# Optimization experiments

Hardware: AMD Instinct MI355X
Metric: run time of the kernel (lower is better)

Reference implementation:

```python
import jax, jax.numpy as jnp
import numpy as np


def setup_inputs() -> dict:
    key = jax.random.key(0)
    k1, k2, k3, k4 = jax.random.split(key, 4)
    b, c, h, w = 4, 256, 64, 64
    Fq_l = jax.random.normal(k1, (b, c, h, w), dtype=jnp.float32)
    Fp_l = jax.random.normal(k2, (b, c, h, w), dtype=jnp.float32)
    # 1x1 conv: weight [out=c//2, in=c], bias [c//2]
    W = jax.random.normal(k3, (c // 2, c), dtype=jnp.float32) * (1.0 / np.sqrt(c))
    bias = jax.random.normal(k4, (c // 2,), dtype=jnp.float32) * 0.01
    return {"Fq_l": Fq_l, "Fp_l": Fp_l, "W": W, "bias": bias}


def reference(Fq_l, Fp_l, W, bias):
    b, c, h, w = Fq_l.shape
    hw = h * w
    # 1x1 conv == per-pixel linear projection
    q = jnp.einsum('oc,bchw->bohw', W, Fq_l) + bias[None, :, None, None]
    p = jnp.einsum('oc,bchw->bohw', W, Fp_l) + bias[None, :, None, None]
    qf = q.reshape(b, -1, hw)  # [b, c/2, hw]
    pf = p.reshape(b, -1, hw)
    qf = qf / jnp.linalg.norm(qf, axis=1, keepdims=True)
    pf = pf / jnp.linalg.norm(pf, axis=1, keepdims=True)
    # cosine similarity, [b, hw, hw]
    sim = jnp.einsum('bcn,bcm->bnm', qf, pf)
    idx = jnp.argmax(sim, axis=-1)  # [b, hw]
    Fp_flat = Fp_l.reshape(b, c, hw)
    aligned = jnp.take_along_axis(Fp_flat, idx[:, None, :], axis=2)  # [b, c, hw]
    return aligned.reshape(b, c, h, w)
```

## Files before the change

kernel.cpp:

```cpp
#include <hip/hip_runtime.h>

#define HW 4096
#define LCAP 1536

typedef short bf16x8 __attribute__((ext_vector_type(8)));
typedef float f32x16 __attribute__((ext_vector_type(16)));

__device__ __forceinline__ ushort f2bf_rne(float f) {
    unsigned u = __float_as_uint(f);
    return (ushort)((u + 0x7FFFu + ((u >> 16) & 1u)) >> 16);
}

__global__ __launch_bounds__(256) void transpose_w_kernel(
    const float* __restrict__ Wm, float* __restrict__ Wt)
{
    const int o = blockIdx.x;
    const int c = threadIdx.x;
    Wt[c * 128 + o] = Wm[o * 256 + c];
}

__global__ __launch_bounds__(256) void proj_kernel(
    const float* __restrict__ Fq, const float* __restrict__ Fp,
    const float* __restrict__ Wt, const float* __restrict__ bias,
    float* __restrict__ Qt, float* __restrict__ Pt,
    ushort* __restrict__ Qpk, ushort* __restrict__ Ppk,
    float* __restrict__ qnorm)
{
    __shared__ float Ws[64][128];
    __shared__ float Xs[64][128];
    __shared__ float psum[16][137];

    const int tid = threadIdx.x;
    const int z  = blockIdx.z;
    const float* __restrict__ X = z ? Fp : Fq;
    const int b  = blockIdx.y;
    const int n0 = blockIdx.x * 128;
    const int og = tid >> 4;
    const int ng = tid & 15;

    float acc[8][8];
    #pragma unroll
    for (int i = 0; i < 8; ++i)
        #pragma unroll
        for (int j = 0; j < 8; ++j) acc[i][j] = 0.f;

    for (int cc = 0; cc < 4; ++cc) {
        __syncthreads();
        {
            const float4* src = (const float4*)(Wt + (size_t)cc * 64 * 128);
            float4* dst = (float4*)Ws;
            #pragma unroll
            for (int it = 0; it < 8; ++it) dst[it * 256 + tid] = src[it * 256 + tid];
        }
        #pragma unroll
        for (int it = 0; it < 8; ++it) {
            int f = it * 256 + tid;
            int r = f >> 5, n4 = f & 31;
            *(float4*)&Xs[r][n4 * 4] =
                *(const float4*)&X[(size_t)(b * 256 + cc * 64 + r) * HW + n0 + n4 * 4];
        }
        __syncthreads();

        for (int r = 0; r < 64; ++r) {
            float4 w0 = *(const float4*)&Ws[r][og * 8];
            float4 w1 = *(const float4*)&Ws[r][og * 8 + 4];
            float4 x0 = *(const float4*)&Xs[r][ng * 8];
            float4 x1 = *(const float4*)&Xs[r][ng * 8 + 4];
            float wa[8] = {w0.x, w0.y, w0.z, w0.w, w1.x, w1.y, w1.z, w1.w};
            float xa[8] = {x0.x, x0.y, x0.z, x0.w, x1.x, x1.y, x1.z, x1.w};
            #pragma unroll
            for (int i = 0; i < 8; ++i)
                #pragma unroll
                for (int j = 0; j < 8; ++j)
                    acc[i][j] += wa[j] * xa[i];
        }
    }

    {
        float4 b0 = *(const float4*)&bias[og * 8];
        float4 b1 = *(const float4*)&bias[og * 8 + 4];
        float ba[8] = {b0.x, b0.y, b0.z, b0.w, b1.x, b1.y, b1.z, b1.w};
        #pragma unroll
        for (int i = 0; i < 8; ++i)
            #pragma unroll
            for (int j = 0; j < 8; ++j) acc[i][j] += ba[j];
    }

    #pragma unroll
    for (int i = 0; i < 8; ++i) {
        float s = 0.f;
        #pragma unroll
        for (int j = 0; j < 8; ++j) s += acc[i][j] * acc[i][j];
        psum[og][ng * 8 + i] = s;
    }
    __syncthreads();
    float tot[8];
    #pragma unroll
    for (int i = 0; i < 8; ++i) {
        float s = 0.f;
        #pragma unroll
        for (int g = 0; g < 16; ++g) s += psum[g][ng * 8 + i];
        tot[i] = s;
    }

    if (z) {
        #pragma unroll
        for (int i = 0; i < 8; ++i) {
            float s = 1.0f / sqrtf(tot[i]);
            #pragma unroll
            for (int j = 0; j < 8; ++j) acc[i][j] *= s;
        }
    } else if (og == 0) {
        #pragma unroll
        for (int i = 0; i < 8; ++i)
            qnorm[b * HW + n0 + ng * 8 + i] = sqrtf(tot[i]);
    }

    {
        float* __restrict__ T = z ? Pt : Qt;
        #pragma unroll
        for (int i = 0; i < 8; ++i) {
            size_t tb = ((size_t)b * HW + n0 + ng * 8 + i) * 128 + og * 8;
            *(float4*)&T[tb]     = make_float4(acc[i][0], acc[i][1], acc[i][2], acc[i][3]);
            *(float4*)&T[tb + 4] = make_float4(acc[i][4], acc[i][5], acc[i][6], acc[i][7]);
        }
    }
    {
        ushort* __restrict__ PK = z ? Ppk : Qpk;
        const int ks = og >> 1;
        #pragma unroll
        for (int i = 0; i < 8; ++i) {
            const int na  = n0 + ng * 8 + i;
            const int t32 = na >> 5;
            const int lt  = (na & 31) + 32 * (og & 1);
            ushort u[8];
            #pragma unroll
            for (int k = 0; k < 8; ++k) u[k] = f2bf_rne(acc[i][k]);
            size_t pk = ((((size_t)b * 128 + t32) * 8 + ks) * 64 + lt) * 8;
            uint4 w;
            w.x = (unsigned)u[0] | ((unsigned)u[1] << 16);
            w.y = (unsigned)u[2] | ((unsigned)u[3] << 16);
            w.z = (unsigned)u[4] | ((unsigned)u[5] << 16);
            w.w = (unsigned)u[6] | ((unsigned)u[7] << 16);
            *(uint4*)&PK[pk] = w;
        }
    }
}

__global__ __launch_bounds__(256, 4) void sim_sketch_kernel(
    const ushort* __restrict__ Qpk, const ushort* __restrict__ Ppk,
    const float* __restrict__ qnorm, unsigned char* __restrict__ SK)
{
    __shared__ ushort Bs[16384];

    const int tid  = threadIdx.x;
    const int lane = tid & 63;
    const int w    = tid >> 6;
    const int nb   = blockIdx.x;
    const int b    = blockIdx.y;
    const int ms   = blockIdx.z;
    const int hi   = lane >> 5;

    {
        const uint4* src = (const uint4*)(Ppk + ((size_t)(b * 128 + ms * 4)) * 4096);
        uint4* dst = (uint4*)Bs;
        #pragma unroll
        for (int it = 0; it < 8; ++it) dst[it * 256 + tid] = src[it * 256 + tid];
    }

    const ushort* __restrict__ qbase =
        Qpk + ((size_t)(b * 128 + nb * 4)) * 4096 + (size_t)lane * 8;
    bf16x8 qf[8];
    #pragma unroll
    for (int ks = 0; ks < 8; ++ks)
        qf[ks] = *(const bf16x8*)(qbase + (w * 8 + ks) * 512);

    float rq[16];
    #pragma unroll
    for (int r = 0; r < 16; ++r) {
        int nl_ = (r & 3) + 8 * (r >> 2) + 4 * hi;
        rq[r] = 256.0f / qnorm[b * HW + nb * 128 + w * 32 + nl_];
    }

    const size_t g16f = (size_t)b * 256 + (size_t)(nb * 4 + w) * 2 + hi;
    const int mb0 = ms * 128 + (lane & 31);

    __syncthreads();

    #pragma unroll 2
    for (int mtl = 0; mtl < 4; ++mtl) {
        f32x16 acc;
        #pragma unroll
        for (int r = 0; r < 16; ++r) acc[r] = 0.f;
        #pragma unroll
        for (int ks = 0; ks < 8; ++ks) {
            bf16x8 bb = *(const bf16x8*)&Bs[((mtl * 8 + ks) * 64 + lane) * 8];
            acc = __builtin_amdgcn_mfma_f32_32x32x16_bf16(qf[ks], bb, acc, 0, 0, 0);
        }

        unsigned dw[4] = {0u, 0u, 0u, 0u};
        #pragma unroll
        for (int r = 0; r < 16; ++r) {
            float x = acc[r] * rq[r];
#if __has_builtin(__builtin_amdgcn_cvt_pk_u8_f32)
            dw[r >> 2] = (unsigned)__builtin_amdgcn_cvt_pk_u8_f32(
                x, (unsigned)(r & 3), (int)dw[r >> 2]);
#else
            int vi = (int)rintf(x);
            vi = vi < 0 ? 0 : (vi > 255 ? 255 : vi);
            dw[r >> 2] |= (unsigned)vi << (8 * (r & 3));
#endif
        }
        const int m = mb0 + mtl * 32;
        uint4 pk;
        pk.x = dw[0]; pk.y = dw[1]; pk.z = dw[2]; pk.w = dw[3];
        *(uint4*)(SK + ((g16f * 4096 + (size_t)m) << 4)) = pk;
    }
}

__device__ __noinline__ void dot_one_slow(
    const float* Qsrow, const float* __restrict__ Pt,
    int b, int m, int n, unsigned long long* __restrict__ best)
{
    const float4* __restrict__ pr = (const float4*)&Pt[((size_t)b * HW + m) * 128];
    float acc = 0.f;
    #pragma unroll
    for (int k = 0; k < 32; ++k) {
        float4 pv = pr[k];
        float4 qv = *(const float4*)&Qsrow[k * 4];
        acc += qv.x * pv.x + qv.y * pv.y + qv.z * pv.z + qv.w * pv.w;
    }
    unsigned u = __float_as_uint(acc);
    unsigned kk = (u & 0x80000000u) ? ~u : (u | 0x80000000u);
    unsigned long long key = ((unsigned long long)kk << 32) | (unsigned)(4095 - m);
    atomicMax(&best[(size_t)b * HW + n], key);
}

__global__ __launch_bounds__(256) void scan_rescore_kernel(
    const unsigned char* __restrict__ SK,
    const float* __restrict__ Qt, const float* __restrict__ Pt,
    unsigned long long* __restrict__ best)
{
    __shared__ float Qs[16][132];
    __shared__ int nlist[16];
    __shared__ int wmax[4][16];
    __shared__ int t8s[16];
    __shared__ ushort hl[LCAP];
    __shared__ unsigned lcnt;

    const int fg  = blockIdx.x;
    const int tid = threadIdx.x;
    const int b = fg >> 8, g = fg & 255, t = g >> 1, gs = g & 1;
    const int wv_ = tid >> 6;

    if (tid == 0) lcnt = 0u;
    if (tid < 16) {
        int n = t * 32 + (tid & 3) + 8 * (tid >> 2) + 4 * gs;
        nlist[tid] = n;
        best[(size_t)b * HW + n] = 0ull;
    }
    __syncthreads();

    #pragma unroll
    for (int it = 0; it < 2; ++it) {
        int idx = it * 256 + tid;
        int row = idx >> 5, c4 = (idx & 31) * 4;
        *(float4*)&Qs[row][c4] =
            *(const float4*)&Qt[((size_t)b * HW + nlist[row]) * 128 + c4];
    }

    const uint4* __restrict__ skrow = (const uint4*)(SK + ((size_t)fg << 16));

    int mx[16];
    #pragma unroll
    for (int j = 0; j < 16; ++j) mx[j] = 0;
    #pragma unroll 4
    for (int it = 0; it < 16; ++it) {
        uint4 v = skrow[it * 256 + tid];
        unsigned wv[4] = {v.x, v.y, v.z, v.w};
        #pragma unroll
        for (int d = 0; d < 4; ++d)
            #pragma unroll
            for (int k = 0; k < 4; ++k)
                mx[d * 4 + k] = max(mx[d * 4 + k], (int)((wv[d] >> (8 * k)) & 255u));
    }
    #pragma unroll
    for (int j = 0; j < 16; ++j) {
        int v = mx[j];
        #pragma unroll
        for (int d = 1; d < 64; d <<= 1)
            v = max(v, __shfl_xor(v, d, 64));
        mx[j] = v;
    }
    if ((tid & 63) == 0) {
        #pragma unroll
        for (int j = 0; j < 16; ++j) wmax[wv_][j] = mx[j];
    }
    __syncthreads();
    if (tid < 16) {
        int m0 = max(max(wmax[0][tid], wmax[1][tid]),
                     max(wmax[2][tid], wmax[3][tid]));
        int tt = m0 - 6;
        t8s[tid] = tt < 0 ? 0 : tt;
    }
    __syncthreads();

    int myt[16];
    #pragma unroll
    for (int j = 0; j < 16; ++j) myt[j] = t8s[j];

    #pragma unroll 4
    for (int it = 0; it < 16; ++it) {
        const int m = it * 256 + tid;
        uint4 v = skrow[it * 256 + tid];
        unsigned wv[4] = {v.x, v.y, v.z, v.w};
        #pragma unroll
        for (int d = 0; d < 4; ++d) {
            #pragma unroll
            for (int k = 0; k < 4; ++k) {
                int bv = (int)((wv[d] >> (8 * k)) & 255u);
                int j = d * 4 + k;
                if (bv >= myt[j]) {
                    unsigned pos = atomicAdd(&lcnt, 1u);
                    if (pos < LCAP) {
                        hl[pos] = (ushort)((j << 12) | m);
                    } else {
                        dot_one_slow(&Qs[j][0], Pt, b, m, nlist[j], best);
                    }
                }
            }
        }
    }

    __syncthreads();
    unsigned cnt = lcnt < LCAP ? lcnt : LCAP;
    for (unsigned p = tid; p < cnt; p += 256) {
        int e = hl[p];
        int j = e >> 12, m = e & 4095;
        const float4* __restrict__ pr = (const float4*)&Pt[((size_t)b * HW + m) * 128];
        float acc = 0.f;
        #pragma unroll
        for (int k = 0; k < 32; ++k) {
            float4 pv = pr[k];
            float4 qv = *(const float4*)&Qs[j][k * 4];
            acc += qv.x * pv.x + qv.y * pv.y + qv.z * pv.z + qv.w * pv.w;
        }
        unsigned u = __float_as_uint(acc);
        unsigned kk = (u & 0x80000000u) ? ~u : (u | 0x80000000u);
        unsigned long long key = ((unsigned long long)kk << 32) | (unsigned)(4095 - m);
        atomicMax(&best[(size_t)b * HW + nlist[j]], key);
    }
}

__global__ __launch_bounds__(256) void gather_kernel(
    const float* __restrict__ Fp, const unsigned long long* __restrict__ best,
    float* __restrict__ out)
{
    __shared__ float row[4096];
    const int blk = blockIdx.x;
    const int c = blk & 255;
    const int b = blk >> 8;
    const int tid = threadIdx.x;

    const float* __restrict__ src = Fp + ((size_t)b * 256 + c) * HW;
    #pragma unroll
    for (int it = 0; it < 4; ++it) {
        int f = it * 256 + tid;
        *(float4*)&row[f * 4] = *(const float4*)&src[f * 4];
    }
    __syncthreads();

    float* __restrict__ dst = out + ((size_t)b * 256 + c) * HW;
    #pragma unroll
    for (int it = 0; it < 16; ++it) {
        int n = it * 256 + tid;
        int m = 4095 - (int)(best[(size_t)b * HW + n] & 0xFFFull);
        dst[n] = row[m];
    }
}

extern "C" void kernel_launch(void* const* d_in, const int* in_sizes, int n_in,
                              void* d_out, int out_size, void* d_ws, size_t ws_size,
                              hipStream_t stream) {
    const float* Fq   = (const float*)d_in[0];
    const float* Fp   = (const float*)d_in[1];
    const float* Wm   = (const float*)d_in[2];
    const float* bias = (const float*)d_in[3];
    float* out = (float*)d_out;

    char* base = (char*)d_ws;
    float*  Qt    = (float*)(base);
    float*  Pt    = (float*)(base + (8u << 20));
    ushort* Qpk   = (ushort*)(base + (16u << 20));
    ushort* Ppk   = (ushort*)(base + (20u << 20));
    unsigned char* SK = (unsigned char*)(base + (24u << 20));
    char* x = base + (88u << 20);
    float*  qnorm = (float*)x;              x += 65536;
    unsigned long long* best = (unsigned long long*)x; x += 131072;
    float*  Wtg   = (float*)x;

    transpose_w_kernel<<<128, 256, 0, stream>>>(Wm, Wtg);
    proj_kernel<<<dim3(32, 4, 2), 256, 0, stream>>>(Fq, Fp, Wtg, bias,
                                                    Qt, Pt, Qpk, Ppk, qnorm);
    sim_sketch_kernel<<<dim3(32, 4, 32), 256, 0, stream>>>(Qpk, Ppk, qnorm, SK);
    scan_rescore_kernel<<<1024, 256, 0, stream>>>(SK, Qt, Pt, best);
    gather_kernel<<<1024, 256, 0, stream>>>(Fp, best, out);
}
```

Before: 179.8 us.

## Register-prefetch next projection chunk and remap pixel columns to avoid LDS conflicts

The projection kernel now loads the next 64-channel chunk of W and X into registers while the current chunk is being computed from shared memory, so global load latency overlaps the FMA loop. Each thread's 8 pixel columns are also split into two groups of 4 (ng*4 and 64+ng*4) instead of 8 contiguous, which is meant to reduce LDS bank conflicts on the X reads. All output index computations are updated to match. The cost is more live registers, and launch bounds are set to one block per SM to allow that.

```diff
diff --git a/kernel.cpp b/kernel.cpp
--- a/kernel.cpp
+++ b/kernel.cpp
@@ -19,7 +19,7 @@
     Wt[c * 128 + o] = Wm[o * 256 + c];
 }
 
-__global__ __launch_bounds__(256) void proj_kernel(
+__global__ __launch_bounds__(256, 1) void proj_kernel(
     const float* __restrict__ Fq, const float* __restrict__ Fp,
     const float* __restrict__ Wt, const float* __restrict__ bias,
     float* __restrict__ Qt, float* __restrict__ Pt,
@@ -44,28 +44,51 @@
         #pragma unroll
         for (int j = 0; j < 8; ++j) acc[i][j] = 0.f;
 
+    float4 wreg[8], xreg[8];
+    {
+        const float4* srcw = (const float4*)(Wt);
+        #pragma unroll
+        for (int it = 0; it < 8; ++it) wreg[it] = srcw[it * 256 + tid];
+        #pragma unroll
+        for (int it = 0; it < 8; ++it) {
+            int f = it * 256 + tid;
+            int r = f >> 5, n4 = f & 31;
+            xreg[it] = *(const float4*)&X[(size_t)(b * 256 + r) * HW + n0 + n4 * 4];
+        }
+    }
+
     for (int cc = 0; cc < 4; ++cc) {
         __syncthreads();
         {
-            const float4* src = (const float4*)(Wt + (size_t)cc * 64 * 128);
             float4* dst = (float4*)Ws;
             #pragma unroll
-            for (int it = 0; it < 8; ++it) dst[it * 256 + tid] = src[it * 256 + tid];
+            for (int it = 0; it < 8; ++it) dst[it * 256 + tid] = wreg[it];
         }
         #pragma unroll
         for (int it = 0; it < 8; ++it) {
             int f = it * 256 + tid;
             int r = f >> 5, n4 = f & 31;
-            *(float4*)&Xs[r][n4 * 4] =
-                *(const float4*)&X[(size_t)(b * 256 + cc * 64 + r) * HW + n0 + n4 * 4];
+            *(float4*)&Xs[r][n4 * 4] = xreg[it];
         }
         __syncthreads();
+
+        if (cc < 3) {
+            const float4* srcw = (const float4*)(Wt + (size_t)(cc + 1) * 64 * 128);
+            #pragma unroll
+            for (int it = 0; it < 8; ++it) wreg[it] = srcw[it * 256 + tid];
+            #pragma unroll
+            for (int it = 0; it < 8; ++it) {
+                int f = it * 256 + tid;
+                int r = f >> 5, n4 = f & 31;
+                xreg[it] = *(const float4*)&X[(size_t)(b * 256 + (cc + 1) * 64 + r) * HW + n0 + n4 * 4];
+            }
+        }
 
         for (int r = 0; r < 64; ++r) {
             float4 w0 = *(const float4*)&Ws[r][og * 8];
             float4 w1 = *(const float4*)&Ws[r][og * 8 + 4];
-            float4 x0 = *(const float4*)&Xs[r][ng * 8];
-            float4 x1 = *(const float4*)&Xs[r][ng * 8 + 4];
+            float4 x0 = *(const float4*)&Xs[r][ng * 4];
+            float4 x1 = *(const float4*)&Xs[r][64 + ng * 4];
             float wa[8] = {w0.x, w0.y, w0.z, w0.w, w1.x, w1.y, w1.z, w1.w};
             float xa[8] = {x0.x, x0.y, x0.z, x0.w, x1.x, x1.y, x1.z, x1.w};
             #pragma unroll
@@ -88,18 +111,20 @@
 
     #pragma unroll
     for (int i = 0; i < 8; ++i) {
+        int col = (i < 4) ? (ng * 4 + i) : (64 + ng * 4 + i - 4);
         float s = 0.f;
         #pragma unroll
         for (int j = 0; j < 8; ++j) s += acc[i][j] * acc[i][j];
-        psum[og][ng * 8 + i] = s;
+        psum[og][col] = s;
     }
     __syncthreads();
     float tot[8];
     #pragma unroll
     for (int i = 0; i < 8; ++i) {
+        int col = (i < 4) ? (ng * 4 + i) : (64 + ng * 4 + i - 4);
         float s = 0.f;
         #pragma unroll
-        for (int g = 0; g < 16; ++g) s += psum[g][ng * 8 + i];
+        for (int g = 0; g < 16; ++g) s += psum[g][col];
         tot[i] = s;
     }
 
@@ -112,15 +137,18 @@
         }
     } else if (og == 0) {
         #pragma unroll
-        for (int i = 0; i < 8; ++i)
-            qnorm[b * HW + n0 + ng * 8 + i] = sqrtf(tot[i]);
+        for (int i = 0; i < 8; ++i) {
+            int col = (i < 4) ? (ng * 4 + i) : (64 + ng * 4 + i - 4);
+            qnorm[b * HW + n0 + col] = sqrtf(tot[i]);
+        }
     }
 
     {
         float* __restrict__ T = z ? Pt : Qt;
         #pragma unroll
         for (int i = 0; i < 8; ++i) {
-            size_t tb = ((size_t)b * HW + n0 + ng * 8 + i) * 128 + og * 8;
+            int col = (i < 4) ? (ng * 4 + i) : (64 + ng * 4 + i - 4);
+            size_t tb = ((size_t)b * HW + n0 + col) * 128 + og * 8;
             *(float4*)&T[tb]     = make_float4(acc[i][0], acc[i][1], acc[i][2], acc[i][3]);
             *(float4*)&T[tb + 4] = make_float4(acc[i][4], acc[i][5], acc[i][6], acc[i][7]);
         }
@@ -130,7 +158,8 @@
         const int ks = og >> 1;
         #pragma unroll
         for (int i = 0; i < 8; ++i) {
-            const int na  = n0 + ng * 8 + i;
+            int col = (i < 4) ? (ng * 4 + i) : (64 + ng * 4 + i - 4);
+            const int na  = n0 + col;
             const int t32 = na >> 5;
             const int lt  = (na & 31) + 32 * (og & 1);
             ushort u[8];
```

Result: slower. 197.1 us (+9.7%).
